# Optimization experiments

Measured on AMD Instinct MI355X. Metric: run time of the kernel, lower is better.

## Reference

```python
import jax, jax.numpy as jnp
import numpy as np

B, S, H, NH = 4, 2048, 1024, 16
D = H // NH  # head dim = 64


def setup_inputs() -> dict:
    key = jax.random.key(0)
    ks = jax.random.split(key, 4)
    scale = 1.0 / np.sqrt(H)
    return {
        "hidden_states": jax.random.normal(ks[0], (B, S, H), dtype=jnp.float32),
        "attention_mask": jnp.zeros((B, 1, 1, S), dtype=jnp.float32),
        "Wq": jax.random.normal(ks[1], (H, H), dtype=jnp.float32) * scale,
        "bq": jnp.zeros((H,), dtype=jnp.float32),
        "Wk": jax.random.normal(ks[2], (H, H), dtype=jnp.float32) * scale,
        "bk": jnp.zeros((H,), dtype=jnp.float32),
        "Wv": jax.random.normal(ks[3], (H, H), dtype=jnp.float32) * scale,
        "bv": jnp.zeros((H,), dtype=jnp.float32),
    }


def _split_heads(x):
    # [B, S, H] -> [B, NH, S, D]
    return x.reshape(B, S, NH, D).transpose(0, 2, 1, 3)


def reference(hidden_states, attention_mask, Wq, bq, Wk, bk, Wv, bv):
    # NOTE: faithful to source quirk: key/value projections are applied to the
    # query projection output (mixed_query_layer), not to keyvalue_states.
    mixed_q = hidden_states @ Wq.T + bq            # [B, S, H]
    q = _split_heads(mixed_q)                       # [B, NH, S, D]
    k = _split_heads(mixed_q @ Wk.T + bk)           # [B, NH, S, D]
    v = _split_heads(mixed_q @ Wv.T + bv)           # [B, NH, S, D]

    scores = jnp.einsum("bhqd,bhkd->bhqk", q, k) / jnp.sqrt(jnp.float32(D))
    scores = scores + attention_mask                # additive mask [B,1,1,S]
    probs = jax.nn.softmax(scores, axis=-1)         # dropout = identity (eval)
    ctx = jnp.einsum("bhqk,bhkd->bhqd", probs, v)   # [B, NH, S, D]
    ctx = ctx.transpose(0, 2, 1, 3).reshape(B, S, H)
    return ctx
```

## Files before the change

### kernel.cpp

```cpp
#include <hip/hip_runtime.h>
#include <stdint.h>

typedef float  f32x4  __attribute__((ext_vector_type(4)));
typedef float  f32x16 __attribute__((ext_vector_type(16)));
typedef short  s16x8  __attribute__((ext_vector_type(8)));
typedef unsigned int u32x4 __attribute__((ext_vector_type(4)));
typedef unsigned short u16;
typedef u16    u16x4 __attribute__((ext_vector_type(4)));

#define SLEN 2048
#define HDIM 1024
#define NHEAD 16
#define DHEAD 64
#define BATCH 4
#define LOG2E 1.44269504088896340736f
#define SC2   0.18033688011111772f
#define ISC2  5.5451774444795623f

__device__ __forceinline__ u16 f2bf(float f) {
  uint32_t u = __builtin_bit_cast(uint32_t, f);
  u += 0x7FFFu + ((u >> 16) & 1u);
  return (u16)(u >> 16);
}

__device__ __forceinline__ uint32_t cvtpk2(float a, float b) {
  uint32_t r;
  asm("v_cvt_pk_bf16_f32 %0, %1, %2" : "=v"(r) : "v"(a), "v"(b));
  return r;
}

__device__ __forceinline__ void gld_lds16(const void* g, void* l) {
  __builtin_amdgcn_global_load_lds(
      (const __attribute__((address_space(1))) unsigned int*)g,
      (__attribute__((address_space(3))) unsigned int*)l, 16, 0, 0);
}

__global__ __launch_bounds__(256) void prep_all(
    const float4* __restrict__ hs, const float4* __restrict__ W0,
    const float4* __restrict__ W1, const float4* __restrict__ W2,
    const float* __restrict__ mask, const float* __restrict__ bq,
    u16* __restrict__ HSb, u16* __restrict__ O0, u16* __restrict__ O1,
    u16* __restrict__ O2, float* __restrict__ m2, float* __restrict__ bqs,
    float* __restrict__ flagp) {
  const int bid = blockIdx.x, tid = threadIdx.x;
  if (bid < 8192) {
    int i = bid * 256 + tid;
    float4 v = hs[i];
    u16x4 o;
    o.x = f2bf(v.x); o.y = f2bf(v.y); o.z = f2bf(v.z); o.w = f2bf(v.w);
    *(u16x4*)(HSb + (size_t)i * 4) = o;
  } else if (bid < 11264) {
    int zz = (bid - 8192) >> 10;
    int i = ((bid - 8192) & 1023) * 256 + tid;
    const float4* in = zz == 0 ? W0 : (zz == 1 ? W1 : W2);
    u16* out = zz == 0 ? O0 : (zz == 1 ? O1 : O2);
    const float sc = zz == 0 ? SC2 : ISC2;
    float4 v = in[i];
    u16x4 o;
    o.x = f2bf(v.x * sc); o.y = f2bf(v.y * sc);
    o.z = f2bf(v.z * sc); o.w = f2bf(v.w * sc);
    *(u16x4*)(out + (size_t)i * 4) = o;
  } else if (bid < 11296) {
    int i = (bid - 11264) * 256 + tid;
    m2[i] = mask[i] * LOG2E;
  } else if (bid < 11297) {
#pragma unroll
    for (int k = 0; k < 4; ++k) bqs[tid + k * 256] = bq[tid + k * 256] * SC2;
  } else {
    float a = 0.f;
#pragma unroll
    for (int k = 0; k < 32; ++k) a += __builtin_fabsf(mask[tid + k * 256]);
    int nz = __any(a != 0.f) ? 1 : 0;
    if ((tid & 63) == 0) flagp[tid >> 6] = (float)nz;
  }
}

__device__ __forceinline__ void gemm_body(const u16* __restrict__ A,
                                          const u16* __restrict__ W,
                                          const float* __restrict__ bias,
                                          u16* __restrict__ C, int mode) {
  __shared__ u16 As[128 * 64];
  __shared__ u16 Bs[128 * 64];
  const int tid = threadIdx.x;
  const int lane = tid & 63;
  const int w = tid >> 6;
  const int wr = w >> 1, wc = w & 1;
  const int brow = blockIdx.y * 128;
  const int bcol = blockIdx.x * 128;
  const int l15 = lane & 15, l4 = lane >> 4;
  const int koff = l4 * 8;

  f32x4 acc[4][4];
#pragma unroll
  for (int m = 0; m < 4; ++m)
#pragma unroll
    for (int n = 0; n < 4; ++n) acc[m][n] = f32x4{0.f, 0.f, 0.f, 0.f};

  for (int kt = 0; kt < HDIM / 64; ++kt) {
    __syncthreads();
#pragma unroll
    for (int it = 0; it < 4; ++it) {
      int c = tid + it * 256;
      int r = c >> 3, c8 = c & 7;
      gld_lds16(A + (size_t)(brow + r) * HDIM + kt * 64 + c8 * 8,
                (u16*)As + (size_t)c * 8);
      gld_lds16(W + (size_t)(bcol + r) * HDIM + kt * 64 + c8 * 8,
                (u16*)Bs + (size_t)c * 8);
    }
    __syncthreads();

#pragma unroll
    for (int kk = 0; kk < 2; ++kk) {
      s16x8 af[4], bfr[4];
#pragma unroll
      for (int m = 0; m < 4; ++m)
        af[m] = *(const s16x8*)(As + (size_t)(wr * 64 + m * 16 + l15) * 64 +
                                kk * 32 + koff);
#pragma unroll
      for (int n = 0; n < 4; ++n)
        bfr[n] = *(const s16x8*)(Bs + (size_t)(wc * 64 + n * 16 + l15) * 64 +
                                 kk * 32 + koff);
#pragma unroll
      for (int m = 0; m < 4; ++m)
#pragma unroll
        for (int n = 0; n < 4; ++n)
          acc[m][n] = __builtin_amdgcn_mfma_f32_16x16x32_bf16(af[m], bfr[n],
                                                              acc[m][n], 0, 0, 0);
    }
  }

#pragma unroll
  for (int n = 0; n < 4; ++n) {
    int col = bcol + wc * 64 + n * 16 + l15;
    float bv = bias[col];
#pragma unroll
    for (int m = 0; m < 4; ++m) {
      int row0 = brow + wr * 64 + m * 16 + l4 * 4;
      if (mode == 0) {
#pragma unroll
        for (int j = 0; j < 4; ++j)
          C[(size_t)(row0 + j) * HDIM + col] = f2bf(acc[m][n][j] + bv);
      } else {
        u16x4 o;
#pragma unroll
        for (int j = 0; j < 4; ++j) o[j] = f2bf(acc[m][n][j] + bv);
        *(u16x4*)(C + (size_t)(((row0 >> 11) << 10) + col) * SLEN +
                  (row0 & (SLEN - 1))) = o;
      }
    }
  }
}

__global__ __launch_bounds__(256) void gemm_bt(const u16* __restrict__ A,
                                               const u16* __restrict__ W,
                                               const float* __restrict__ bias,
                                               u16* __restrict__ C) {
  gemm_body(A, W, bias, C, 0);
}

__global__ __launch_bounds__(256) void gemm_kv(const u16* __restrict__ A,
                                               const u16* __restrict__ Wk,
                                               const float* __restrict__ bk,
                                               u16* __restrict__ K,
                                               const u16* __restrict__ Wv,
                                               const float* __restrict__ bv,
                                               u16* __restrict__ Vt) {
  if (blockIdx.z == 0) gemm_body(A, Wk, bk, K, 0);
  else                 gemm_body(A, Wv, bv, Vt, 1);
}

__global__ __launch_bounds__(256, 4) void attn_kernel(
    const u16* __restrict__ Qs, const u16* __restrict__ Kb,
    const u16* __restrict__ Vtg, const float* __restrict__ m2g,
    const float* __restrict__ flagp, float* __restrict__ out) {
  __shared__ u16 Ks[2][64 * 64];
  __shared__ u16 Vts[2][64 * 64];

  const int tid = threadIdx.x;
  const int lane = tid & 63;
  const int w = tid >> 6;
  const int bid = blockIdx.x;
  const int swz = (bid & 7) * 128 + (bid >> 3);
  const int qt = swz & 15;
  const int bh = swz >> 4;
  const int b = bh >> 4, h = bh & 15;
  const int l31 = lane & 31;
  const int h1 = lane >> 5;

  const float4 fl = *(const float4*)flagp;
  const bool mz = (fl.x == 0.f && fl.y == 0.f && fl.z == 0.f && fl.w == 0.f);

  const int q0 = qt * 128 + w * 32;
  s16x8 qf[4];
  {
    const u16* qp = Qs + (size_t)(b * SLEN + q0 + l31) * HDIM + h * DHEAD + h1 * 8;
#pragma unroll
    for (int dch = 0; dch < 4; ++dch) qf[dch] = *(const s16x8*)(qp + dch * 16);
  }

  const s16x8 onesf = {(short)0x3F80, (short)0x3F80, (short)0x3F80,
                       (short)0x3F80, (short)0x3F80, (short)0x3F80,
                       (short)0x3F80, (short)0x3F80};

  const float zf = fl.x * 0.0f;
  f32x16 zc;
#pragma unroll
  for (int i = 0; i < 16; ++i) zc[i] = zf;

  const int r0 = tid >> 3, c0 = tid & 7;
  const int cl0 = c0 ^ (r0 & 7);
  const int r1 = r0 + 32;
  const int cl1 = c0 ^ (r1 & 7);
  const u16* Kbase = Kb + (size_t)(b * SLEN) * HDIM + h * DHEAD;
  const u16* Vbase = Vtg + (size_t)bh * 64 * SLEN;
  const float* mbase = m2g + b * SLEN;
  const u16* KstA = Kbase + (size_t)r0 * HDIM + cl0 * 8;
  const u16* KstB = Kbase + (size_t)r1 * HDIM + cl1 * 8;
  const u16* VstA = Vbase + (size_t)r0 * SLEN + cl0 * 8;
  const u16* VstB = Vbase + (size_t)r1 * SLEN + cl1 * 8;

  f32x16 acc0{}, acc1{}, acc_s{};

  auto stage = [&](u16* Kd, u16* Vd, int kbn) {
    const size_t ko = (size_t)kbn * 64 * HDIM;
    const int vo = kbn * 64;
    gld_lds16(KstA + ko, Kd + tid * 8);
    gld_lds16(KstB + ko, Kd + (tid + 256) * 8);
    gld_lds16(VstA + vo, Vd + tid * 8);
    gld_lds16(VstB + vo, Vd + (tid + 256) * 8);
  };

  auto tile = [&](const u16* Kc, const u16* Vc, int kb) {
    uint32_t W[16];
#pragma unroll
    for (int kblk = 0; kblk < 2; ++kblk) {
      f32x16 cinit;
      if (mz) {
        cinit = zc;
      } else {
#pragma unroll
        for (int g = 0; g < 4; ++g) {
          float4 mk =
              *(const float4*)(mbase + kb * 64 + kblk * 32 + g * 8 + h1 * 4);
          cinit[4 * g + 0] = mk.x; cinit[4 * g + 1] = mk.y;
          cinit[4 * g + 2] = mk.z; cinit[4 * g + 3] = mk.w;
        }
      }
      const int row = kblk * 32 + l31;
      __builtin_amdgcn_s_setprio(1);
      f32x16 sT;
      {
        const int ch = h1 ^ (row & 7);
        s16x8 kf = *(const s16x8*)(Kc + row * 64 + ch * 8);
        sT = __builtin_amdgcn_mfma_f32_32x32x16_bf16(kf, qf[0], cinit, 0, 0, 0);
      }
#pragma unroll
      for (int dch = 1; dch < 4; ++dch) {
        const int ch = (dch * 2 + h1) ^ (row & 7);
        s16x8 kf = *(const s16x8*)(Kc + row * 64 + ch * 8);
        sT = __builtin_amdgcn_mfma_f32_32x32x16_bf16(kf, qf[dch], sT, 0, 0, 0);
      }
      __builtin_amdgcn_s_setprio(0);
#pragma unroll
      for (int g = 0; g < 4; ++g) {
        float p0 = __builtin_amdgcn_exp2f(sT[4 * g + 0]);
        float p1 = __builtin_amdgcn_exp2f(sT[4 * g + 1]);
        float p2 = __builtin_amdgcn_exp2f(sT[4 * g + 2]);
        float p3 = __builtin_amdgcn_exp2f(sT[4 * g + 3]);
        W[kblk * 8 + 2 * g]     = cvtpk2(p0, p1);
        W[kblk * 8 + 2 * g + 1] = cvtpk2(p2, p3);
      }
    }

#pragma unroll
    for (int c = 0; c < 4; ++c) {
#pragma unroll
      for (int e = 0; e < 2; ++e) {
        uint32_t a = W[4 * c + e], bb = W[4 * c + 2 + e];
        asm("v_permlane32_swap_b32 %0, %1" : "+v"(a), "+v"(bb));
        W[4 * c + e] = a;
        W[4 * c + 2 + e] = bb;
      }
    }

    __builtin_amdgcn_s_setprio(1);
#pragma unroll
    for (int c = 0; c < 4; ++c) {
      u32x4 t = {W[4 * c], W[4 * c + 1], W[4 * c + 2], W[4 * c + 3]};
      s16x8 af = __builtin_bit_cast(s16x8, t);
      const int ch = (c * 2 + h1) ^ (l31 & 7);
      s16x8 vf0 = *(const s16x8*)(Vc + l31 * 64 + ch * 8);
      s16x8 vf1 = *(const s16x8*)(Vc + (32 + l31) * 64 + ch * 8);
      acc0 = __builtin_amdgcn_mfma_f32_32x32x16_bf16(af, vf0, acc0, 0, 0, 0);
      acc1 = __builtin_amdgcn_mfma_f32_32x32x16_bf16(af, vf1, acc1, 0, 0, 0);
      acc_s = __builtin_amdgcn_mfma_f32_32x32x16_bf16(af, onesf, acc_s, 0, 0, 0);
    }
    __builtin_amdgcn_s_setprio(0);
  };

  stage(&Ks[0][0], &Vts[0][0], 0);
  __syncthreads();

#pragma unroll 1
  for (int t = 0; t < 15; ++t) {
    stage(&Ks[1][0], &Vts[1][0], 2 * t + 1);
    tile(&Ks[0][0], &Vts[0][0], 2 * t);
    __syncthreads();
    stage(&Ks[0][0], &Vts[0][0], 2 * t + 2);
    tile(&Ks[1][0], &Vts[1][0], 2 * t + 1);
    __syncthreads();
  }
  stage(&Ks[1][0], &Vts[1][0], 31);
  tile(&Ks[0][0], &Vts[0][0], 30);
  __syncthreads();
  tile(&Ks[1][0], &Vts[1][0], 31);

  const size_t obase = (size_t)(b * SLEN + q0);
#pragma unroll
  for (int r = 0; r < 16; ++r) {
    const int qr = (r & 3) + 8 * (r >> 2) + 4 * h1;
    const float si = 1.0f / acc_s[r];
    float* op = out + (obase + qr) * HDIM + h * DHEAD;
    op[l31]      = acc0[r] * si;
    op[32 + l31] = acc1[r] * si;
  }
}

extern "C" void kernel_launch(void* const* d_in, const int* in_sizes, int n_in,
                              void* d_out, int out_size, void* d_ws, size_t ws_size,
                              hipStream_t stream) {
  (void)in_sizes; (void)n_in; (void)out_size; (void)ws_size;
  const float* hs   = (const float*)d_in[0];
  const float* mask = (const float*)d_in[1];
  const float* Wq   = (const float*)d_in[2];
  const float* bq   = (const float*)d_in[3];
  const float* Wk   = (const float*)d_in[4];
  const float* bk   = (const float*)d_in[5];
  const float* Wv   = (const float*)d_in[6];
  const float* bv   = (const float*)d_in[7];
  float* out = (float*)d_out;

  char* ws = (char*)d_ws;
  const size_t MTOK = (size_t)BATCH * SLEN;
  const size_t MB = 1024 * 1024;
  u16* HSb = (u16*)ws;
  u16* Wqs = (u16*)(ws + 16 * MB);
  u16* Wks = (u16*)(ws + 18 * MB);
  u16* Wvs = (u16*)(ws + 20 * MB);
  u16* Qs  = (u16*)(ws + 22 * MB);
  u16* Kb  = (u16*)(ws + 38 * MB);
  u16* Vt  = (u16*)(ws + 54 * MB);
  float* m2  = (float*)(ws + 70 * MB);
  float* bqs = m2 + MTOK;
  float* flg = bqs + 1024;

  prep_all<<<11298, 256, 0, stream>>>((const float4*)hs, (const float4*)Wq,
                                      (const float4*)Wk, (const float4*)Wv,
                                      mask, bq, HSb, Wqs, Wks, Wvs, m2, bqs, flg);

  dim3 gg(HDIM / 128, MTOK / 128);
  gemm_bt<<<gg, 256, 0, stream>>>(HSb, Wqs, bqs, Qs);
  dim3 gkv(HDIM / 128, MTOK / 128, 2);
  gemm_kv<<<gkv, 256, 0, stream>>>(Qs, Wks, bk, Kb, Wvs, bv, Vt);

  attn_kernel<<<BATCH * NHEAD * (SLEN / 128), 256, 0, stream>>>(Qs, Kb, Vt, m2,
                                                                flg, out);
}
```

Before: 187.9 us.

## Pipeline GEMM projection with 4-slot LDS ring, XOR swizzle, and block-order remap

Rewrites the projection GEMM main loop to stream K in 32-wide stages through a 4-deep LDS ring. Loads run three stages ahead, gated by explicit vmcnt waits and a single barrier per stage instead of two syncthreads. It also XOR-swizzles LDS columns to reduce bank conflicts and remaps block indices so co-resident blocks share A/W tiles in L2. The cost is hand-tuned waitcnt counts that depend on the exact number of outstanding loads. The single-barrier ring reuse also relies on the slot being overwritten not yet being read.

After: 172.2 us. 8.3% less time.

```diff
diff --git a/kernel.cpp b/kernel.cpp
--- a/kernel.cpp
+++ b/kernel.cpp
@@ -79,16 +79,24 @@
                                           const u16* __restrict__ W,
                                           const float* __restrict__ bias,
                                           u16* __restrict__ C, int mode) {
-  __shared__ u16 As[128 * 64];
-  __shared__ u16 Bs[128 * 64];
+  __shared__ u16 As[4][128 * 32];
+  __shared__ u16 Bs[4][128 * 32];
   const int tid = threadIdx.x;
   const int lane = tid & 63;
   const int w = tid >> 6;
   const int wr = w >> 1, wc = w & 1;
-  const int brow = blockIdx.y * 128;
-  const int bcol = blockIdx.x * 128;
+  const int flat = blockIdx.x + blockIdx.y * 8;
+  const int swz = (flat & 7) * 64 + (flat >> 3);
+  const int brow = (swz >> 3) * 128;
+  const int bcol = (swz & 7) * 128;
   const int l15 = lane & 15, l4 = lane >> 4;
-  const int koff = l4 * 8;
+
+  const int r0 = tid >> 2, c0 = tid & 3;
+  const int sc0 = c0 ^ ((r0 >> 1) & 3);
+  const int r1 = r0 + 64;
+  const int sc1 = c0 ^ ((r1 >> 1) & 3);
+  const u16* Abase = A + (size_t)brow * HDIM;
+  const u16* Bbase = W + (size_t)bcol * HDIM;
 
   f32x4 acc[4][4];
 #pragma unroll
@@ -96,38 +104,55 @@
 #pragma unroll
     for (int n = 0; n < 4; ++n) acc[m][n] = f32x4{0.f, 0.f, 0.f, 0.f};
 
-  for (int kt = 0; kt < HDIM / 64; ++kt) {
-    __syncthreads();
-#pragma unroll
-    for (int it = 0; it < 4; ++it) {
-      int c = tid + it * 256;
-      int r = c >> 3, c8 = c & 7;
-      gld_lds16(A + (size_t)(brow + r) * HDIM + kt * 64 + c8 * 8,
-                (u16*)As + (size_t)c * 8);
-      gld_lds16(W + (size_t)(bcol + r) * HDIM + kt * 64 + c8 * 8,
-                (u16*)Bs + (size_t)c * 8);
-    }
-    __syncthreads();
-
-#pragma unroll
-    for (int kk = 0; kk < 2; ++kk) {
-      s16x8 af[4], bfr[4];
-#pragma unroll
-      for (int m = 0; m < 4; ++m)
-        af[m] = *(const s16x8*)(As + (size_t)(wr * 64 + m * 16 + l15) * 64 +
-                                kk * 32 + koff);
+  auto stage = [&](int s) {
+    const int slot = s & 3;
+    const int k0 = s * 32;
+    gld_lds16(Abase + (size_t)r0 * HDIM + k0 + sc0 * 8, &As[slot][tid * 8]);
+    gld_lds16(Abase + (size_t)r1 * HDIM + k0 + sc1 * 8,
+              &As[slot][(tid + 256) * 8]);
+    gld_lds16(Bbase + (size_t)r0 * HDIM + k0 + sc0 * 8, &Bs[slot][tid * 8]);
+    gld_lds16(Bbase + (size_t)r1 * HDIM + k0 + sc1 * 8,
+              &Bs[slot][(tid + 256) * 8]);
+  };
+
+  auto compute = [&](int s) {
+    const int slot = s & 3;
+    s16x8 af[4], bf[4];
+#pragma unroll
+    for (int m = 0; m < 4; ++m) {
+      const int row = wr * 64 + m * 16 + l15;
+      const int pc = l4 ^ ((row >> 1) & 3);
+      af[m] = *(const s16x8*)&As[slot][row * 32 + pc * 8];
+    }
+#pragma unroll
+    for (int n = 0; n < 4; ++n) {
+      const int row = wc * 64 + n * 16 + l15;
+      const int pc = l4 ^ ((row >> 1) & 3);
+      bf[n] = *(const s16x8*)&Bs[slot][row * 32 + pc * 8];
+    }
+    if (s < 29) stage(s + 3);
+#pragma unroll
+    for (int m = 0; m < 4; ++m)
 #pragma unroll
       for (int n = 0; n < 4; ++n)
-        bfr[n] = *(const s16x8*)(Bs + (size_t)(wc * 64 + n * 16 + l15) * 64 +
-                                 kk * 32 + koff);
-#pragma unroll
-      for (int m = 0; m < 4; ++m)
-#pragma unroll
-        for (int n = 0; n < 4; ++n)
-          acc[m][n] = __builtin_amdgcn_mfma_f32_16x16x32_bf16(af[m], bfr[n],
-                                                              acc[m][n], 0, 0, 0);
-    }
-  }
+        acc[m][n] = __builtin_amdgcn_mfma_f32_16x16x32_bf16(af[m], bf[n],
+                                                            acc[m][n], 0, 0, 0);
+  };
+
+  stage(0); stage(1); stage(2);
+
+#pragma unroll 1
+  for (int s = 0; s < 30; ++s) {
+    asm volatile("s_waitcnt vmcnt(8)" ::: "memory");
+    asm volatile("s_barrier" ::: "memory");
+    compute(s);
+  }
+  asm volatile("s_waitcnt vmcnt(4)" ::: "memory");
+  asm volatile("s_barrier" ::: "memory");
+  compute(30);
+  asm volatile("s_waitcnt vmcnt(0)" ::: "memory");
+  asm volatile("s_barrier" ::: "memory");
+  compute(31);
 
 #pragma unroll
   for (int n = 0; n < 4; ++n) {
```
